# Performance work log

Measured on AMD Instinct MI355X. Metric: run time of the kernel, lower is better.

Reference implementation:

```python
import jax, jax.numpy as jnp
import numpy as np

# state constants (mirroring e_state/v_state/t_state dicts from __init__)
E_SCALE = 1000.0
E_INIT = 5000.0
V_SCALE = 1.0
V_INIT = 1.0
T_INIT = 500.0
T_DELTA = 50.0
T_DELTA_SCALE = 1.0

EULER = 0.5772156649015329
# Abramowitz & Stegun 5.1.56 rational approx for x*e^x*E1(x), x >= 1
_A = (8.5733287401, 18.0590169730, 8.6347608925, 0.2677737343)
_B = (9.5733223454, 25.6329561486, 21.0996530827, 3.9584969228)


def _expi_impl(z):
    # Ei(z) for z < 0 via Ei(-x) = -E1(x), x = -z > 0
    x = -z
    # small-x branch: E1(x) = -gamma - ln x + sum_{k>=1} (-1)^{k+1} x^k/(k*k!)
    xs = jnp.clip(x, 1e-30, 1.0)
    term = jnp.ones_like(xs)
    s = jnp.zeros_like(xs)
    for k in range(1, 26):  # 25 terms: converged to fp32 precision for x<=1
        term = term * (-xs) / k
        s = s + term / k
    small = EULER + jnp.log(xs) + s  # = -E1(x) negated -> Ei(-x)
    # large-x branch: E1(x) ~ exp(-x)/x * P(x)/Q(x)
    xl = jnp.maximum(x, 1.0)
    a1, a2, a3, a4 = _A
    b1, b2, b3, b4 = _B
    P = (((xl + a1) * xl + a2) * xl + a3) * xl + a4
    Q = (((xl + b1) * xl + b2) * xl + b3) * xl + b4
    large = -(jnp.exp(-xl) / xl) * (P / Q)
    return jnp.where(x <= 1.0, small, large)


@jax.custom_vjp
def expi(z):
    return _expi_impl(z)


def _expi_fwd(z):
    return _expi_impl(z), z


def _expi_bwd(z, g):
    # matches the torch custom backward: d/dz Ei(z) = exp(z)/z, with safe z
    safe = jnp.where(jnp.abs(z) < 1e-10, jnp.full_like(z, 1e-10), z)
    return (g * jnp.exp(safe) / safe,)


expi.defvjp(_expi_fwd, _expi_bwd)


def setup_inputs() -> dict:
    key = jax.random.key(0)
    N = 16777216  # 2^24 temperature samples (~64 MB fp32)
    temps = 300.0 + 500.0 * jax.random.uniform(key, (N,), dtype=jnp.float32)
    return {
        "input": temps,
        "global_shift": jnp.zeros((1,), jnp.float32),
        "E_param": jnp.array([np.log(E_INIT / E_SCALE)], jnp.float32),
        "T_max_delta": jnp.zeros((1,), jnp.float32),
        "V_max": jnp.array([np.log(V_INIT / V_SCALE)], jnp.float32),
    }


def reference(input, global_shift, E_param, T_max_delta, V_max):
    # model == 'second' branch of OxideModel.forward
    E = jnp.clip(jnp.exp(E_param) * E_SCALE, 1e-10, 1e10)      # [1]
    V = jnp.clip(jnp.exp(V_max) * V_SCALE, 1e-10, 1e10)        # [1]
    T_max = T_INIT + T_DELTA * jnp.tanh(T_max_delta * T_DELTA_SCALE) + global_shift
    sT = jnp.maximum(T_max, 1e-10)                              # [1]
    st = jnp.maximum(input, 1e-10)                              # [N]
    U = jnp.sqrt(V)
    K = E / sT + (2.0 / 3.0) * jnp.log(1.5 * E * U / sT ** 2)   # [1]

    def f(t):
        return K - E / t

    def integral(t):
        return jnp.exp(K) * (t * jnp.exp(-E / t) + E * expi(-E / t))

    result = integral(st) - integral(sT)                        # [N]
    exp_arg = jnp.clip(f(st) - f(sT), -100.0, 100.0)            # [N]
    inner = U - (1.0 / 3.0) * jnp.exp(f(sT) / 2.0) * result     # [N]
    return jnp.exp(exp_arg) * jnp.maximum(inner, 0.0) ** 2      # relu2
```

## Files before the change

kernel.cpp:

```cpp
#include <hip/hip_runtime.h>
#include <math.h>


struct Scalars {
    float E;
    float U;
    float K;
    float expK;
    float xT;
    float fsT;
    float coef;
    float IsT;
};

__device__ __forceinline__ float expi_negx(float x, float e) {
    if (x <= 1.0f) {
        float xs = fminf(fmaxf(x, 1e-30f), 1.0f);
        float term = 1.0f;
        float s = 0.0f;
#pragma unroll 1
        for (int k = 1; k <= 25; ++k) {
            term = term * (-xs) / (float)k;
            s += term / (float)k;
        }
        return 0.5772156649015329f + logf(xs) + s;
    } else {
        float P = (((x + 8.5733287401f) * x + 18.0590169730f) * x + 8.6347608925f) * x
                  + 0.2677737343f;
        float Q = (((x + 9.5733223454f) * x + 25.6329561486f) * x + 21.0996530827f) * x
                  + 3.9584969228f;
        return -(e / x) * (P / Q);
    }
}

__device__ __forceinline__ Scalars make_scalars(float gshift, float E_param,
                                                float T_max_delta, float V_max) {
    Scalars s;
    s.E = fminf(fmaxf(expf(E_param) * 1000.0f, 1e-10f), 1e10f);
    float V = fminf(fmaxf(expf(V_max) * 1.0f, 1e-10f), 1e10f);
    float T_max = 500.0f + 50.0f * tanhf(T_max_delta * 1.0f) + gshift;
    float sT = fmaxf(T_max, 1e-10f);
    s.U = sqrtf(V);
    s.K = s.E / sT + (2.0f / 3.0f) * logf(1.5f * s.E * s.U / (sT * sT));
    s.expK = expf(s.K);
    s.xT = s.E / sT;
    s.fsT = s.K - s.xT;
    s.coef = (1.0f / 3.0f) * expf(s.fsT * 0.5f);
    float eT = expf(-s.xT);
    float eiT = expi_negx(s.xT, eT);
    s.IsT = s.expK * (sT * eT + s.E * eiT);
    return s;
}

__device__ __forceinline__ float compute_one(float t, const Scalars& s) {
    float st = fmaxf(t, 1e-10f);
    float x = s.E / st;
    float e = expf(-x);
    float ei = expi_negx(x, e);
    float Ist = s.expK * (st * e + s.E * ei);
    float result = Ist - s.IsT;
    float exp_arg = (s.K - x) - s.fsT;
    exp_arg = fminf(fmaxf(exp_arg, -100.0f), 100.0f);
    float inner = s.U - s.coef * result;
    float r = fmaxf(inner, 0.0f);
    return expf(exp_arg) * (r * r);
}

extern "C" __global__ void __launch_bounds__(256, 4)
oxide_kernel(const float* __restrict__ in,
             const float* __restrict__ p_gs,
             const float* __restrict__ p_E,
             const float* __restrict__ p_Td,
             const float* __restrict__ p_V,
             float* __restrict__ out, int n) {
    Scalars s = make_scalars(p_gs[0], p_E[0], p_Td[0], p_V[0]);

    int tid = blockIdx.x * blockDim.x + threadIdx.x;
    int stride = gridDim.x * blockDim.x;
    int n4 = n >> 2;
    const float4* __restrict__ in4 = (const float4*)in;
    float4* __restrict__ out4 = (float4*)out;

    for (int i = tid; i < n4; i += stride) {
        float4 v = in4[i];
        float4 o;
        o.x = compute_one(v.x, s);
        o.y = compute_one(v.y, s);
        o.z = compute_one(v.z, s);
        o.w = compute_one(v.w, s);
        out4[i] = o;
    }
    int base = n4 << 2;
    for (int i = base + tid; i < n; i += stride) {
        out[i] = compute_one(in[i], s);
    }
}

extern "C" void kernel_launch(void* const* d_in, const int* in_sizes, int n_in,
                              void* d_out, int out_size, void* d_ws, size_t ws_size,
                              hipStream_t stream) {
    const float* in = (const float*)d_in[0];
    const float* gs = (const float*)d_in[1];
    const float* Ep = (const float*)d_in[2];
    const float* Td = (const float*)d_in[3];
    const float* Vm = (const float*)d_in[4];
    float* out = (float*)d_out;
    int n = in_sizes[0];

    const int threads = 256;
    const int blocks = 2048;
    oxide_kernel<<<blocks, threads, 0, stream>>>(in, gs, Ep, Td, Vm, out, n);
}
```

Baseline: 135.1 us.

## Fold expi large-x branch into a single rational and hoist scalar constants

```diff
diff --git a/kernel.cpp b/kernel.cpp
--- a/kernel.cpp
+++ b/kernel.cpp
@@ -3,67 +3,78 @@
 
 
 struct Scalars {
-    float E;
-    float U;
-    float K;
-    float expK;
-    float xT;
-    float fsT;
-    float coef;
-    float IsT;
+    float E, U, K, expK, coef, fsT, IsT;
+    float A;
+    float B;
+    float C;
 };
 
-__device__ __forceinline__ float expi_negx(float x, float e) {
-    if (x <= 1.0f) {
-        float xs = fminf(fmaxf(x, 1e-30f), 1.0f);
-        float term = 1.0f;
-        float s = 0.0f;
-#pragma unroll 1
-        for (int k = 1; k <= 25; ++k) {
-            term = term * (-xs) / (float)k;
-            s += term / (float)k;
-        }
-        return 0.5772156649015329f + logf(xs) + s;
-    } else {
-        float P = (((x + 8.5733287401f) * x + 18.0590169730f) * x + 8.6347608925f) * x
-                  + 0.2677737343f;
-        float Q = (((x + 9.5733223454f) * x + 25.6329561486f) * x + 21.0996530827f) * x
-                  + 3.9584969228f;
-        return -(e / x) * (P / Q);
-    }
+__device__ __forceinline__ float poly_N(float x) {
+    return fmaf(fmaf(fmaf(0.9999936053f, x, 7.5739391756f), x, 12.4648921902f),
+                x, 3.6907231885f);
+}
+__device__ __forceinline__ float poly_Q(float x) {
+    return fmaf(fmaf(fmaf((x + 9.5733223454f), x, 25.6329561486f), x,
+                     21.0996530827f), x, 3.9584969228f);
 }
 
 __device__ __forceinline__ Scalars make_scalars(float gshift, float E_param,
                                                 float T_max_delta, float V_max) {
     Scalars s;
     s.E = fminf(fmaxf(expf(E_param) * 1000.0f, 1e-10f), 1e10f);
-    float V = fminf(fmaxf(expf(V_max) * 1.0f, 1e-10f), 1e10f);
-    float T_max = 500.0f + 50.0f * tanhf(T_max_delta * 1.0f) + gshift;
+    float V = fminf(fmaxf(expf(V_max), 1e-10f), 1e10f);
+    float T_max = 500.0f + 50.0f * tanhf(T_max_delta) + gshift;
     float sT = fmaxf(T_max, 1e-10f);
     s.U = sqrtf(V);
-    s.K = s.E / sT + (2.0f / 3.0f) * logf(1.5f * s.E * s.U / (sT * sT));
+    float xT = s.E / sT;
+    s.K = xT + (2.0f / 3.0f) * logf(1.5f * s.E * s.U / (sT * sT));
     s.expK = expf(s.K);
-    s.xT = s.E / sT;
-    s.fsT = s.K - s.xT;
+    s.fsT = s.K - xT;
     s.coef = (1.0f / 3.0f) * expf(s.fsT * 0.5f);
-    float eT = expf(-s.xT);
-    float eiT = expi_negx(s.xT, eT);
-    s.IsT = s.expK * (sT * eT + s.E * eiT);
+    float eT = expf(-xT);
+    if (xT > 1.0f) {
+        s.IsT = s.expK * sT * eT * (poly_N(xT) / poly_Q(xT));
+    } else {
+        float xs = fminf(fmaxf(xT, 1e-30f), 1.0f);
+        float term = 1.0f, acc = 0.0f;
+#pragma unroll 1
+        for (int k = 1; k <= 25; ++k) {
+            term = term * (-xs) / (float)k;
+            acc += term / (float)k;
+        }
+        float ei = 0.5772156649015329f + logf(xs) + acc;
+        s.IsT = s.expK * (sT * eT + s.E * ei);
+    }
+    s.A = expf(xT);
+    s.B = s.coef * s.expK;
+    s.C = s.U + s.coef * s.IsT;
     return s;
 }
 
 __device__ __forceinline__ float compute_one(float t, const Scalars& s) {
     float st = fmaxf(t, 1e-10f);
-    float x = s.E / st;
-    float e = expf(-x);
-    float ei = expi_negx(x, e);
-    float Ist = s.expK * (st * e + s.E * ei);
-    float result = Ist - s.IsT;
-    float exp_arg = (s.K - x) - s.fsT;
-    exp_arg = fminf(fmaxf(exp_arg, -100.0f), 100.0f);
-    float inner = s.U - s.coef * result;
+    float x = s.E * __builtin_amdgcn_rcpf(st);
+    float e = __builtin_amdgcn_exp2f(x * -1.44269504088896f);
+    if (x <= 1.0f) {
+        float xs = fminf(fmaxf(x, 1e-30f), 1.0f);
+        float term = 1.0f, acc = 0.0f;
+#pragma unroll 1
+        for (int k = 1; k <= 25; ++k) {
+            term = term * (-xs) / (float)k;
+            acc += term / (float)k;
+        }
+        float ei = 0.5772156649015329f + logf(xs) + acc;
+        float e2 = expf(-x);
+        float Ist = s.expK * (st * e2 + s.E * ei);
+        float exp_arg = fminf(fmaxf((s.K - x) - s.fsT, -100.0f), 100.0f);
+        float inner = s.U - s.coef * (Ist - s.IsT);
+        float r = fmaxf(inner, 0.0f);
+        return expf(exp_arg) * r * r;
+    }
+    float R = poly_N(x) * __builtin_amdgcn_rcpf(poly_Q(x));
+    float inner = fmaf(-s.B * (st * e), R, s.C);
     float r = fmaxf(inner, 0.0f);
-    return expf(exp_arg) * (r * r);
+    return (s.A * e) * (r * r);
 }
 
 extern "C" __global__ void __launch_bounds__(256, 4)
```

Result: faster. 121.0 us (-10.4%).
